# Performance work log

Hardware: AMD Instinct MI355X
Metric: run time of the kernel (lower is better)

## Reference

```python
import jax, jax.numpy as jnp
import numpy as np

D_MODEL = 1024
N_HEADS = 16
DEPTH = D_MODEL // N_HEADS
NEG_INF = -1.0e9


def setup_inputs() -> dict:
    key = jax.random.key(0)
    ks = jax.random.split(key, 11)
    B, S = 2, 2048
    xk = jax.random.normal(ks[0], (B, S, D_MODEL), jnp.float32)
    xq = jax.random.normal(ks[1], (B, S, D_MODEL), jnp.float32)
    xv = jax.random.normal(ks[2], (B, S, D_MODEL), jnp.float32)
    sc = 1.0 / np.sqrt(D_MODEL)
    wq = jax.random.normal(ks[3], (D_MODEL, D_MODEL), jnp.float32) * sc
    wk = jax.random.normal(ks[4], (D_MODEL, D_MODEL), jnp.float32) * sc
    wv = jax.random.normal(ks[5], (D_MODEL, D_MODEL), jnp.float32) * sc
    wo = jax.random.normal(ks[6], (D_MODEL, D_MODEL), jnp.float32) * sc
    bq = jnp.zeros((D_MODEL,), jnp.float32)
    bk = jnp.zeros((D_MODEL,), jnp.float32)
    bv = jnp.zeros((D_MODEL,), jnp.float32)
    bo = jnp.zeros((D_MODEL,), jnp.float32)
    return {"xk": xk, "xq": xq, "xv": xv, "wq": wq, "bq": bq, "wk": wk,
            "bk": bk, "wv": wv, "bv": bv, "wo": wo, "bo": bo}


def _split_heads(t):
    # [B, S, D] -> [B, H, S, depth]
    B, S, _ = t.shape
    return t.reshape(B, S, N_HEADS, DEPTH).transpose(0, 2, 1, 3)


def reference(xk, xq, xv, wq, bq, wk, bk, wv, bv, wo, bo):
    B, Sq, _ = xq.shape
    Sk = xk.shape[1]
    q = _split_heads(xq @ wq + bq)  # [B,H,Sq,d]
    k = _split_heads(xk @ wk + bk)  # [B,H,Sk,d]
    v = _split_heads(xv @ wv + bv)  # [B,H,Sk,d]
    logits = jnp.einsum('bhqd,bhkd->bhqk', q, k) / jnp.sqrt(
        jnp.asarray(DEPTH, q.dtype))
    # additive causal mask: (1 - lower_triangular) * -1e9
    causal = (1.0 - jnp.tril(jnp.ones((Sq, Sk), logits.dtype))) * NEG_INF
    logits = logits + causal[None, None, :, :]
    attn = jax.nn.softmax(logits, axis=-1)
    out = jnp.einsum('bhqk,bhkd->bhqd', attn, v)
    out = out.transpose(0, 2, 1, 3).reshape(B, Sq, D_MODEL)
    return out @ wo + bo
```

## Files before the change

### kernel.cpp

```cpp
#include <hip/hip_runtime.h>

typedef unsigned short u16;
typedef u16 u16x8 __attribute__((ext_vector_type(8)));
typedef __bf16 bf16x8 __attribute__((ext_vector_type(8)));
typedef float f32x4 __attribute__((ext_vector_type(4)));

#define DM 1024
#define SEQ 2048
#define BATCH 2
#define MROWS 4096

__device__ __forceinline__ u16 f2bf(float f) {
  unsigned int x = __builtin_bit_cast(unsigned int, f);
  x += 0x7fffu + ((x >> 16) & 1u);
  return (u16)(x >> 16);
}
__device__ __forceinline__ u16 f2bf_trunc(float f) {
  return (u16)(__builtin_bit_cast(unsigned int, f) >> 16);
}

__device__ __forceinline__ void gld16(const void* g, void* l) {
  __builtin_amdgcn_global_load_lds(
      (const __attribute__((address_space(1))) void*)g,
      (__attribute__((address_space(3))) void*)l, 16, 0, 0);
}

struct TrArgs { const float* in[4]; u16* out[4]; };

__global__ __launch_bounds__(256) void transpose_w4(TrArgs a) {
  const float* __restrict__ in = a.in[blockIdx.z];
  u16* __restrict__ out = a.out[blockIdx.z];
  __shared__ u16 T[64][72];
  int r0 = blockIdx.y * 64, c0 = blockIdx.x * 64;
  int t = threadIdx.x;
  int r = t >> 3, cg = (t & 7) * 8;
#pragma unroll
  for (int p = 0; p < 2; p++) {
    const float* src = in + (size_t)(r0 + r + p * 32) * DM + c0 + cg;
    f32x4 x0 = *(const f32x4*)src;
    f32x4 x1 = *(const f32x4*)(src + 4);
    u16x8 v;
#pragma unroll
    for (int j = 0; j < 4; j++) { v[j] = f2bf(x0[j]); v[4 + j] = f2bf(x1[j]); }
    *(u16x8*)(&T[r + p * 32][cg]) = v;
  }
  __syncthreads();
#pragma unroll
  for (int p = 0; p < 2; p++) {
    int orow = r + p * 32;
    u16x8 v;
#pragma unroll
    for (int j = 0; j < 8; j++) v[j] = T[cg + j][orow];
    *(u16x8*)(out + (size_t)(c0 + orow) * DM + r0 + cg) = v;
  }
}

struct CastArgs { const float* in[3]; u16* out[3]; };

__global__ __launch_bounds__(256) void cast_x(CastArgs a) {
  const float* __restrict__ in = a.in[blockIdx.y];
  u16* __restrict__ out = a.out[blockIdx.y];
  size_t e = ((size_t)blockIdx.x * 256 + threadIdx.x) * 8;
  f32x4 a0 = *(const f32x4*)(in + e);
  f32x4 a1 = *(const f32x4*)(in + e + 4);
  u16x8 v;
#pragma unroll
  for (int j = 0; j < 4; j++) { v[j] = f2bf(a0[j]); v[4 + j] = f2bf(a1[j]); }
  *(u16x8*)(out + e) = v;
}

struct GemmArgs { const void* A[3]; const u16* WT[3]; const float* bias[3]; void* C[3]; };

template <int MT, int NT, bool AF32, bool OF32>
__global__ __launch_bounds__(256) void gemmT(GemmArgs g) {
  __shared__ __align__(16) u16 As[MT * 32 * 32];
  __shared__ __align__(16) u16 Bs[NT * 32 * 32];
  const int z = blockIdx.z;
  const u16* __restrict__ WT = g.WT[z];
  const int tid = threadIdx.x;
  const int lane = tid & 63, wave = tid >> 6;
  const int fr = lane & 15, kq = lane >> 4;
  const int mq = (wave >> 1) * (MT * 16), nq = (wave & 1) * (NT * 16);
  const int m0 = blockIdx.y * (MT * 32), n0 = blockIdx.x * (NT * 32);
  const int srow = tid >> 2;
  const int scA = ((tid & 3) ^ ((srow >> 1) & 3)) * 8;
  const int fco = ((kq ^ ((fr >> 1) & 3)) * 8);
  f32x4 acc[MT][NT] = {};

  for (int kk = 0; kk < DM; kk += 32) {
    __syncthreads();
    if constexpr (AF32) {
      const float* A = (const float*)g.A[z];
#pragma unroll
      for (int i = 0; i < MT / 2; i++) {
        const float* s0 = A + (size_t)(m0 + i * 64 + srow) * DM + kk + scA;
        f32x4 a0 = *(const f32x4*)s0, a1 = *(const f32x4*)(s0 + 4);
        u16x8 v;
#pragma unroll
        for (int j = 0; j < 4; j++) { v[j] = f2bf(a0[j]); v[4 + j] = f2bf(a1[j]); }
        *(u16x8*)(As + (i * 256 + tid) * 8) = v;
      }
    } else {
      const u16* A = (const u16*)g.A[z];
#pragma unroll
      for (int i = 0; i < MT / 2; i++)
        gld16(A + (size_t)(m0 + i * 64 + srow) * DM + kk + scA,
              As + (i * 256 + tid) * 8);
    }
#pragma unroll
    for (int i = 0; i < NT / 2; i++)
      gld16(WT + (size_t)(n0 + i * 64 + srow) * DM + kk + scA,
            Bs + (i * 256 + tid) * 8);
    __syncthreads();
    bf16x8 af[MT], bfr[NT];
#pragma unroll
    for (int mt = 0; mt < MT; mt++)
      af[mt] = __builtin_bit_cast(
          bf16x8, *(const u16x8*)(As + (mq + mt * 16 + fr) * 32 + fco));
#pragma unroll
    for (int nt = 0; nt < NT; nt++)
      bfr[nt] = __builtin_bit_cast(
          bf16x8, *(const u16x8*)(Bs + (nq + nt * 16 + fr) * 32 + fco));
#pragma unroll
    for (int mt = 0; mt < MT; mt++)
#pragma unroll
      for (int nt = 0; nt < NT; nt++)
        acc[mt][nt] =
            __builtin_amdgcn_mfma_f32_16x16x32_bf16(af[mt], bfr[nt], acc[mt][nt], 0, 0, 0);
  }
  const float* __restrict__ bias = g.bias[z];
#pragma unroll
  for (int nt = 0; nt < NT; nt++) {
    int col = n0 + nq + nt * 16 + fr;
    float bb = bias[col];
#pragma unroll
    for (int mt = 0; mt < MT; mt++)
#pragma unroll
      for (int r = 0; r < 4; r++) {
        int row = m0 + mq + mt * 16 + kq * 4 + r;
        float val = acc[mt][nt][r] + bb;
        if constexpr (OF32)
          ((float*)g.C[z])[(size_t)row * DM + col] = val;
        else
          ((u16*)g.C[z])[(size_t)row * DM + col] = f2bf(val);
      }
  }
}

#define KS 72
__global__ __launch_bounds__(256) void attn3(u16* __restrict__ Q,
                                             const u16* __restrict__ K,
                                             const u16* __restrict__ V) {
  __shared__ __align__(16) u16 Ksh[64 * 64];
  __shared__ __align__(16) u16 Vt[80 * KS];
  __shared__ __align__(16) u16 Ps[4][16 * KS];
  const int tid = threadIdx.x, wave = tid >> 6, lane = tid & 63;
  const int fr = lane & 15, kq = lane >> 4;
  const int b = blockIdx.x >> 4, h = blockIdx.x & 15;
  const int qt = 31 - blockIdx.y;
  const float C1 = 0.125f * 1.44269504f;

#pragma unroll
  for (int i = 0; i < 4; i++) {
    int e = tid * 4 + i;
    int rr = e >> 6, cc = e & 63;
    Vt[(64 + rr) * KS + cc] = (rr == 0) ? (u16)0x3F80 : (u16)0;
  }

  const int krow = tid >> 3;
  const int kcs = ((tid & 7) ^ (krow & 7)) * 8;
  const int f7 = fr & 7;
  const int x0 = (kq ^ f7) * 8;
  const int x1 = ((4 + kq) ^ f7) * 8;

  bf16x8 qf0, qf1;
  {
    size_t qr = (size_t)(b * SEQ + qt * 64 + wave * 16 + fr) * DM + h * 64;
    qf0 = __builtin_bit_cast(bf16x8, *(const u16x8*)(Q + qr + kq * 8));
    qf1 = __builtin_bit_cast(bf16x8, *(const u16x8*)(Q + qr + 32 + kq * 8));
  }

  f32x4 ov[5] = {};
  u16* Pw = Ps[wave];

  for (int t = 0; t <= qt; t++) {
    __syncthreads();
    {
      size_t gk = (size_t)(b * SEQ + t * 64 + krow) * DM + h * 64 + kcs;
      gld16(K + gk, Ksh + tid * 8);
      gld16(K + gk + (size_t)32 * DM, Ksh + (256 + tid) * 8);
      size_t gv = (size_t)(b * SEQ + t * 64 + lane) * DM + h * 64 + wave * 16;
      u16x8 v0 = *(const u16x8*)(V + gv);
      u16x8 v1 = *(const u16x8*)(V + gv + 8);
#pragma unroll
      for (int j = 0; j < 8; j++) {
        Vt[(wave * 16 + j) * KS + lane] = v0[j];
        Vt[(wave * 16 + 8 + j) * KS + lane] = v1[j];
      }
    }
    __syncthreads();
    f32x4 sv[4];
#pragma unroll
    for (int nt = 0; nt < 4; nt++) {
      f32x4 s = {};
      bf16x8 b0 = __builtin_bit_cast(
          bf16x8, *(const u16x8*)(Ksh + (nt * 16 + fr) * 64 + x0));
      s = __builtin_amdgcn_mfma_f32_16x16x32_bf16(qf0, b0, s, 0, 0, 0);
      bf16x8 b1 = __builtin_bit_cast(
          bf16x8, *(const u16x8*)(Ksh + (nt * 16 + fr) * 64 + x1));
      s = __builtin_amdgcn_mfma_f32_16x16x32_bf16(qf1, b1, s, 0, 0, 0);
      sv[nt] = s;
    }
    if (t == qt) {
#pragma unroll
      for (int nt = 0; nt < 4; nt++)
#pragma unroll
        for (int r = 0; r < 4; r++)
          if (nt * 16 + fr > wave * 16 + kq * 4 + r) sv[nt][r] = -1e30f;
    }
#pragma unroll
    for (int nt = 0; nt < 4; nt++)
#pragma unroll
      for (int r = 0; r < 4; r++) {
        float pp = __builtin_amdgcn_exp2f(sv[nt][r] * C1);
        Pw[(kq * 4 + r) * KS + nt * 16 + fr] = f2bf_trunc(pp);
      }
#pragma unroll
    for (int kk = 0; kk < 2; kk++) {
      bf16x8 pa = __builtin_bit_cast(
          bf16x8, *(const u16x8*)(Pw + fr * KS + kk * 32 + kq * 8));
#pragma unroll
      for (int nt = 0; nt < 5; nt++) {
        bf16x8 vb = __builtin_bit_cast(
            bf16x8, *(const u16x8*)(Vt + (nt * 16 + fr) * KS + kk * 32 + kq * 8));
        ov[nt] = __builtin_amdgcn_mfma_f32_16x16x32_bf16(pa, vb, ov[nt], 0, 0, 0);
      }
    }
  }
  float rinv[4];
#pragma unroll
  for (int r = 0; r < 4; r++) rinv[r] = 1.0f / __shfl(ov[4][r], lane & 48);
#pragma unroll
  for (int nt = 0; nt < 4; nt++)
#pragma unroll
    for (int r = 0; r < 4; r++) {
      int row = qt * 64 + wave * 16 + kq * 4 + r;
      Q[(size_t)(b * SEQ + row) * DM + h * 64 + nt * 16 + fr] =
          f2bf(ov[nt][r] * rinv[r]);
    }
}

extern "C" void kernel_launch(void* const* d_in, const int* in_sizes, int n_in,
                              void* d_out, int out_size, void* d_ws,
                              size_t ws_size, hipStream_t stream) {
  const float* xk = (const float*)d_in[0];
  const float* xq = (const float*)d_in[1];
  const float* xv = (const float*)d_in[2];
  const float* wq = (const float*)d_in[3];
  const float* bq = (const float*)d_in[4];
  const float* wk = (const float*)d_in[5];
  const float* bk = (const float*)d_in[6];
  const float* wv = (const float*)d_in[7];
  const float* bv = (const float*)d_in[8];
  const float* wo = (const float*)d_in[9];
  const float* bo = (const float*)d_in[10];

  u16* Qb = (u16*)d_ws;
  u16* Kb = Qb + (size_t)MROWS * DM;
  u16* Vb = Kb + (size_t)MROWS * DM;
  u16* WTq = Vb + (size_t)MROWS * DM;
  u16* WTk = WTq + (size_t)DM * DM;
  u16* WTv = WTk + (size_t)DM * DM;
  u16* WTo = WTv + (size_t)DM * DM;
  u16* Xq = WTo + (size_t)DM * DM;
  u16* Xk = Xq + (size_t)MROWS * DM;
  u16* Xv = Xk + (size_t)MROWS * DM;
  const bool cast_path =
      ws_size >= ((size_t)(3 * 8 + 4 * 2 + 3 * 8)) * 1024 * 1024;

  dim3 blk(256);

  TrArgs tr;
  tr.in[0] = wq; tr.in[1] = wk; tr.in[2] = wv; tr.in[3] = wo;
  tr.out[0] = WTq; tr.out[1] = WTk; tr.out[2] = WTv; tr.out[3] = WTo;
  transpose_w4<<<dim3(16, 16, 4), blk, 0, stream>>>(tr);

  GemmArgs gq;
  gq.WT[0] = WTq; gq.WT[1] = WTk; gq.WT[2] = WTv;
  gq.bias[0] = bq; gq.bias[1] = bk; gq.bias[2] = bv;
  gq.C[0] = Qb; gq.C[1] = Kb; gq.C[2] = Vb;
  if (cast_path) {
    CastArgs ca;
    ca.in[0] = xq; ca.in[1] = xk; ca.in[2] = xv;
    ca.out[0] = Xq; ca.out[1] = Xk; ca.out[2] = Xv;
    cast_x<<<dim3(MROWS * DM / 2048, 3), blk, 0, stream>>>(ca);
    gq.A[0] = Xq; gq.A[1] = Xk; gq.A[2] = Xv;
    gemmT<4, 4, false, false>
        <<<dim3(DM / 128, MROWS / 128, 3), blk, 0, stream>>>(gq);
  } else {
    gq.A[0] = xq; gq.A[1] = xk; gq.A[2] = xv;
    gemmT<4, 4, true, false>
        <<<dim3(DM / 128, MROWS / 128, 3), blk, 0, stream>>>(gq);
  }

  attn3<<<dim3(BATCH * 16, 32), blk, 0, stream>>>(Qb, Kb, Vb);

  GemmArgs go;
  go.A[0] = Qb;  go.WT[0] = WTo; go.bias[0] = bo; go.C[0] = d_out;
  go.A[1] = Qb;  go.WT[1] = WTo; go.bias[1] = bo; go.C[1] = d_out;
  go.A[2] = Qb;  go.WT[2] = WTo; go.bias[2] = bo; go.C[2] = d_out;
  gemmT<2, 4, false, true>
      <<<dim3(DM / 128, MROWS / 64, 1), blk, 0, stream>>>(go);
}
```

Before: 224.1 us.

## Emit transposed V from projection GEMM and restructure attention to 128-thread blocks

The QKV projection GEMM now uses a configurable K-tile (64) and writes V directly in a per-head transposed layout. The attention kernel can then load V with async global-to-LDS copies instead of scalar LDS transposes. The attention kernel is rewritten with 2 waves, each handling 32 query rows. It computes S^T so probabilities can be packed with perm into LDS, and it accumulates row sums with shuffles instead of an extra ones-column in V. The output GEMM is retiled to 64x64 blocks. The trade-offs are scattered 2-byte strided stores for transposed V and fewer threads per attention block.

```diff
diff --git a/kernel.cpp b/kernel.cpp
--- a/kernel.cpp
+++ b/kernel.cpp
@@ -1,7 +1,9 @@
 #include <hip/hip_runtime.h>
 
 typedef unsigned short u16;
+typedef unsigned int u32;
 typedef u16 u16x8 __attribute__((ext_vector_type(8)));
+typedef u32 u32x2 __attribute__((ext_vector_type(2)));
 typedef __bf16 bf16x8 __attribute__((ext_vector_type(8)));
 typedef float f32x4 __attribute__((ext_vector_type(4)));
 
@@ -15,8 +17,10 @@
   x += 0x7fffu + ((x >> 16) & 1u);
   return (u16)(x >> 16);
 }
-__device__ __forceinline__ u16 f2bf_trunc(float f) {
-  return (u16)(__builtin_bit_cast(unsigned int, f) >> 16);
+
+__device__ __forceinline__ u32 pack2bf(float lo, float hi) {
+  return __builtin_amdgcn_perm(__builtin_bit_cast(u32, hi),
+                               __builtin_bit_cast(u32, lo), 0x07060302u);
 }
 
 __device__ __forceinline__ void gld16(const void* g, void* l) {
@@ -71,64 +75,77 @@
 
 struct GemmArgs { const void* A[3]; const u16* WT[3]; const float* bias[3]; void* C[3]; };
 
-template <int MT, int NT, bool AF32, bool OF32>
+template <int MT, int NT, int BK, bool AF32, bool OF32, bool VT>
 __global__ __launch_bounds__(256) void gemmT(GemmArgs g) {
-  __shared__ __align__(16) u16 As[MT * 32 * 32];
-  __shared__ __align__(16) u16 Bs[NT * 32 * 32];
+  constexpr int CH = BK / 8;
+  constexpr int CM = CH - 1;
+  constexpr int SH = (CH == 4) ? 1 : 0;
+  __shared__ __align__(16) u16 As[MT * 32 * BK];
+  __shared__ __align__(16) u16 Bs[NT * 32 * BK];
   const int z = blockIdx.z;
   const u16* __restrict__ WT = g.WT[z];
-  const int tid = threadIdx.x;
-  const int lane = tid & 63, wave = tid >> 6;
+  const int tid = threadIdx.x, lane = tid & 63, wave = tid >> 6;
   const int fr = lane & 15, kq = lane >> 4;
   const int mq = (wave >> 1) * (MT * 16), nq = (wave & 1) * (NT * 16);
   const int m0 = blockIdx.y * (MT * 32), n0 = blockIdx.x * (NT * 32);
-  const int srow = tid >> 2;
-  const int scA = ((tid & 3) ^ ((srow >> 1) & 3)) * 8;
-  const int fco = ((kq ^ ((fr >> 1) & 3)) * 8);
+  const int fsel = (fr >> SH) & CM;
   f32x4 acc[MT][NT] = {};
 
-  for (int kk = 0; kk < DM; kk += 32) {
+  for (int kk = 0; kk < DM; kk += BK) {
     __syncthreads();
+    constexpr int AI = MT * 32 * CH / 256;
+    constexpr int BI = NT * 32 * CH / 256;
     if constexpr (AF32) {
       const float* A = (const float*)g.A[z];
 #pragma unroll
-      for (int i = 0; i < MT / 2; i++) {
-        const float* s0 = A + (size_t)(m0 + i * 64 + srow) * DM + kk + scA;
+      for (int i = 0; i < AI; i++) {
+        int ci = i * 256 + tid, row = ci / CH, sl = ci % CH;
+        int sc = (sl ^ ((row >> SH) & CM)) * 8;
+        const float* s0 = A + (size_t)(m0 + row) * DM + kk + sc;
         f32x4 a0 = *(const f32x4*)s0, a1 = *(const f32x4*)(s0 + 4);
         u16x8 v;
 #pragma unroll
         for (int j = 0; j < 4; j++) { v[j] = f2bf(a0[j]); v[4 + j] = f2bf(a1[j]); }
-        *(u16x8*)(As + (i * 256 + tid) * 8) = v;
+        *(u16x8*)(As + ci * 8) = v;
       }
     } else {
       const u16* A = (const u16*)g.A[z];
 #pragma unroll
-      for (int i = 0; i < MT / 2; i++)
-        gld16(A + (size_t)(m0 + i * 64 + srow) * DM + kk + scA,
-              As + (i * 256 + tid) * 8);
-    }
-#pragma unroll
-    for (int i = 0; i < NT / 2; i++)
-      gld16(WT + (size_t)(n0 + i * 64 + srow) * DM + kk + scA,
-            Bs + (i * 256 + tid) * 8);
+      for (int i = 0; i < AI; i++) {
+        int ci = i * 256 + tid, row = ci / CH, sl = ci % CH;
+        int sc = (sl ^ ((row >> SH) & CM)) * 8;
+        gld16(A + (size_t)(m0 + row) * DM + kk + sc, As + ci * 8);
+      }
+    }
+#pragma unroll
+    for (int i = 0; i < BI; i++) {
+      int ci = i * 256 + tid, row = ci / CH, sl = ci % CH;
+      int sc = (sl ^ ((row >> SH) & CM)) * 8;
+      gld16(WT + (size_t)(n0 + row) * DM + kk + sc, Bs + ci * 8);
+    }
     __syncthreads();
-    bf16x8 af[MT], bfr[NT];
-#pragma unroll
-    for (int mt = 0; mt < MT; mt++)
-      af[mt] = __builtin_bit_cast(
-          bf16x8, *(const u16x8*)(As + (mq + mt * 16 + fr) * 32 + fco));
-#pragma unroll
-    for (int nt = 0; nt < NT; nt++)
-      bfr[nt] = __builtin_bit_cast(
-          bf16x8, *(const u16x8*)(Bs + (nq + nt * 16 + fr) * 32 + fco));
-#pragma unroll
-    for (int mt = 0; mt < MT; mt++)
+#pragma unroll
+    for (int kc = 0; kc < BK / 32; kc++) {
+      bf16x8 af[MT], bfr[NT];
+      const int fo = ((kc * 4 + kq) ^ fsel) * 8;
+#pragma unroll
+      for (int mt = 0; mt < MT; mt++)
+        af[mt] = __builtin_bit_cast(
+            bf16x8, *(const u16x8*)(As + (mq + mt * 16 + fr) * BK + fo));
 #pragma unroll
       for (int nt = 0; nt < NT; nt++)
-        acc[mt][nt] =
-            __builtin_amdgcn_mfma_f32_16x16x32_bf16(af[mt], bfr[nt], acc[mt][nt], 0, 0, 0);
+        bfr[nt] = __builtin_bit_cast(
+            bf16x8, *(const u16x8*)(Bs + (nq + nt * 16 + fr) * BK + fo));
+#pragma unroll
+      for (int mt = 0; mt < MT; mt++)
+#pragma unroll
+        for (int nt = 0; nt < NT; nt++)
+          acc[mt][nt] = __builtin_amdgcn_mfma_f32_16x16x32_bf16(
+              af[mt], bfr[nt], acc[mt][nt], 0, 0, 0);
+    }
   }
   const float* __restrict__ bias = g.bias[z];
+  const bool vtr = VT && (z == 2);
 #pragma unroll
   for (int nt = 0; nt < NT; nt++) {
     int col = n0 + nq + nt * 16 + fr;
@@ -139,115 +156,156 @@
       for (int r = 0; r < 4; r++) {
         int row = m0 + mq + mt * 16 + kq * 4 + r;
         float val = acc[mt][nt][r] + bb;
-        if constexpr (OF32)
+        if constexpr (OF32) {
           ((float*)g.C[z])[(size_t)row * DM + col] = val;
-        else
-          ((u16*)g.C[z])[(size_t)row * DM + col] = f2bf(val);
-      }
-  }
-}
-
-#define KS 72
-__global__ __launch_bounds__(256) void attn3(u16* __restrict__ Q,
+        } else {
+          u16* C = (u16*)g.C[z];
+          if (vtr) {
+            size_t idx = ((size_t)((row >> 11) * 16 + (col >> 6)) * 64 +
+                          (col & 63)) * SEQ + (row & 2047);
+            C[idx] = f2bf(val);
+          } else {
+            C[(size_t)row * DM + col] = f2bf(val);
+          }
+        }
+      }
+  }
+}
+
+__global__ __launch_bounds__(128) void attn4(u16* __restrict__ Q,
                                              const u16* __restrict__ K,
-                                             const u16* __restrict__ V) {
+                                             const u16* __restrict__ Vtg) {
   __shared__ __align__(16) u16 Ksh[64 * 64];
-  __shared__ __align__(16) u16 Vt[80 * KS];
-  __shared__ __align__(16) u16 Ps[4][16 * KS];
-  const int tid = threadIdx.x, wave = tid >> 6, lane = tid & 63;
-  const int fr = lane & 15, kq = lane >> 4;
-  const int b = blockIdx.x >> 4, h = blockIdx.x & 15;
+  __shared__ __align__(16) u16 Vsh[64 * 64];
+  __shared__ __align__(16) u16 Psh[64 * 64];
+  __shared__ float Lbuf[2][32];
+  const int tid = threadIdx.x, wq = tid >> 6, lane = tid & 63;
+  const int fr = lane & 15, kq = lane >> 4, f7 = fr & 7;
+  const int bh = blockIdx.x, b = bh >> 4, h = bh & 15;
   const int qt = 31 - blockIdx.y;
   const float C1 = 0.125f * 1.44269504f;
 
+  int xo[2];
+  xo[0] = (kq ^ f7) * 8;
+  xo[1] = ((4 + kq) ^ f7) * 8;
+
+  const u16* kp[4];
+  const u16* vp[4];
 #pragma unroll
   for (int i = 0; i < 4; i++) {
-    int e = tid * 4 + i;
-    int rr = e >> 6, cc = e & 63;
-    Vt[(64 + rr) * KS + cc] = (rr == 0) ? (u16)0x3F80 : (u16)0;
-  }
-
-  const int krow = tid >> 3;
-  const int kcs = ((tid & 7) ^ (krow & 7)) * 8;
-  const int f7 = fr & 7;
-  const int x0 = (kq ^ f7) * 8;
-  const int x1 = ((4 + kq) ^ f7) * 8;
-
-  bf16x8 qf0, qf1;
-  {
-    size_t qr = (size_t)(b * SEQ + qt * 64 + wave * 16 + fr) * DM + h * 64;
-    qf0 = __builtin_bit_cast(bf16x8, *(const u16x8*)(Q + qr + kq * 8));
-    qf1 = __builtin_bit_cast(bf16x8, *(const u16x8*)(Q + qr + 32 + kq * 8));
-  }
-
-  f32x4 ov[5] = {};
-  u16* Pw = Ps[wave];
+    int ci = i * 128 + tid, row = ci >> 3, sl = ci & 7;
+    int sc = (sl ^ (row & 7)) * 8;
+    kp[i] = K + (size_t)(b * SEQ + row) * DM + h * 64 + sc;
+    vp[i] = Vtg + (size_t)(bh * 64 + row) * SEQ + sc;
+  }
+
+  bf16x8 qf[2][2];
+#pragma unroll
+  for (int qtl = 0; qtl < 2; qtl++) {
+    size_t qr = (size_t)(b * SEQ + qt * 64 + wq * 32 + qtl * 16 + fr) * DM + h * 64;
+#pragma unroll
+    for (int kk = 0; kk < 2; kk++)
+      qf[qtl][kk] =
+          __builtin_bit_cast(bf16x8, *(const u16x8*)(Q + qr + kk * 32 + kq * 8));
+  }
+
+  f32x4 ov[2][4] = {};
+  float lac[2] = {0.f, 0.f};
 
   for (int t = 0; t <= qt; t++) {
     __syncthreads();
-    {
-      size_t gk = (size_t)(b * SEQ + t * 64 + krow) * DM + h * 64 + kcs;
-      gld16(K + gk, Ksh + tid * 8);
-      gld16(K + gk + (size_t)32 * DM, Ksh + (256 + tid) * 8);
-      size_t gv = (size_t)(b * SEQ + t * 64 + lane) * DM + h * 64 + wave * 16;
-      u16x8 v0 = *(const u16x8*)(V + gv);
-      u16x8 v1 = *(const u16x8*)(V + gv + 8);
-#pragma unroll
-      for (int j = 0; j < 8; j++) {
-        Vt[(wave * 16 + j) * KS + lane] = v0[j];
-        Vt[(wave * 16 + 8 + j) * KS + lane] = v1[j];
-      }
+#pragma unroll
+    for (int i = 0; i < 4; i++) {
+      int ci = i * 128 + tid;
+      gld16(kp[i] + (size_t)t * 64 * DM, Ksh + ci * 8);
+      gld16(vp[i] + t * 64, Vsh + ci * 8);
     }
     __syncthreads();
-    f32x4 sv[4];
-#pragma unroll
-    for (int nt = 0; nt < 4; nt++) {
-      f32x4 s = {};
-      bf16x8 b0 = __builtin_bit_cast(
-          bf16x8, *(const u16x8*)(Ksh + (nt * 16 + fr) * 64 + x0));
-      s = __builtin_amdgcn_mfma_f32_16x16x32_bf16(qf0, b0, s, 0, 0, 0);
-      bf16x8 b1 = __builtin_bit_cast(
-          bf16x8, *(const u16x8*)(Ksh + (nt * 16 + fr) * 64 + x1));
-      s = __builtin_amdgcn_mfma_f32_16x16x32_bf16(qf1, b1, s, 0, 0, 0);
-      sv[nt] = s;
+
+    f32x4 st[2][4];
+#pragma unroll
+    for (int kt = 0; kt < 4; kt++) {
+      bf16x8 k0 = __builtin_bit_cast(
+          bf16x8, *(const u16x8*)(Ksh + (kt * 16 + fr) * 64 + xo[0]));
+      bf16x8 k1 = __builtin_bit_cast(
+          bf16x8, *(const u16x8*)(Ksh + (kt * 16 + fr) * 64 + xo[1]));
+#pragma unroll
+      for (int qtl = 0; qtl < 2; qtl++) {
+        f32x4 s = {};
+        s = __builtin_amdgcn_mfma_f32_16x16x32_bf16(k0, qf[qtl][0], s, 0, 0, 0);
+        s = __builtin_amdgcn_mfma_f32_16x16x32_bf16(k1, qf[qtl][1], s, 0, 0, 0);
+        st[qtl][kt] = s;
+      }
     }
     if (t == qt) {
 #pragma unroll
-      for (int nt = 0; nt < 4; nt++)
-#pragma unroll
-        for (int r = 0; r < 4; r++)
-          if (nt * 16 + fr > wave * 16 + kq * 4 + r) sv[nt][r] = -1e30f;
-    }
+      for (int qtl = 0; qtl < 2; qtl++)
+#pragma unroll
+        for (int kt = 0; kt < 4; kt++)
+#pragma unroll
+          for (int r = 0; r < 4; r++)
+            if (kt * 16 + kq * 4 + r > wq * 32 + qtl * 16 + fr)
+              st[qtl][kt][r] = -1e30f;
+    }
+#pragma unroll
+    for (int qtl = 0; qtl < 2; qtl++) {
+      float ls = 0.f;
+      int prow = (wq * 32 + qtl * 16 + fr) * 64;
+#pragma unroll
+      for (int kt = 0; kt < 4; kt++) {
+        float p0 = __builtin_amdgcn_exp2f(st[qtl][kt][0] * C1);
+        float p1 = __builtin_amdgcn_exp2f(st[qtl][kt][1] * C1);
+        float p2 = __builtin_amdgcn_exp2f(st[qtl][kt][2] * C1);
+        float p3 = __builtin_amdgcn_exp2f(st[qtl][kt][3] * C1);
+        ls += (p0 + p1) + (p2 + p3);
+        u32x2 d;
+        d[0] = pack2bf(p0, p1);
+        d[1] = pack2bf(p2, p3);
+        int sl = (2 * kt + (kq >> 1)) ^ f7;
+        *(u32x2*)(Psh + prow + sl * 8 + (kq & 1) * 4) = d;
+      }
+      ls += __shfl_xor(ls, 16);
+      ls += __shfl_xor(ls, 32);
+      lac[qtl] += ls;
+    }
+#pragma unroll
+    for (int kk = 0; kk < 2; kk++) {
+      bf16x8 pa[2];
+#pragma unroll
+      for (int qtl = 0; qtl < 2; qtl++)
+        pa[qtl] = __builtin_bit_cast(
+            bf16x8,
+            *(const u16x8*)(Psh + (wq * 32 + qtl * 16 + fr) * 64 + xo[kk]));
+#pragma unroll
+      for (int nt = 0; nt < 4; nt++) {
+        bf16x8 vb = __builtin_bit_cast(
+            bf16x8, *(const u16x8*)(Vsh + (nt * 16 + fr) * 64 + xo[kk]));
+#pragma unroll
+        for (int qtl = 0; qtl < 2; qtl++)
+          ov[qtl][nt] = __builtin_amdgcn_mfma_f32_16x16x32_bf16(
+              pa[qtl], vb, ov[qtl][nt], 0, 0, 0);
+      }
+    }
+  }
+  if (kq == 0) {
+    Lbuf[wq][fr] = lac[0];
+    Lbuf[wq][16 + fr] = lac[1];
+  }
+#pragma unroll
+  for (int qtl = 0; qtl < 2; qtl++) {
+    float rinv[4];
+#pragma unroll
+    for (int r = 0; r < 4; r++)
+      rinv[r] = 1.0f / Lbuf[wq][qtl * 16 + kq * 4 + r];
 #pragma unroll
     for (int nt = 0; nt < 4; nt++)
 #pragma unroll
       for (int r = 0; r < 4; r++) {
-        float pp = __builtin_amdgcn_exp2f(sv[nt][r] * C1);
-        Pw[(kq * 4 + r) * KS + nt * 16 + fr] = f2bf_trunc(pp);
-      }
-#pragma unroll
-    for (int kk = 0; kk < 2; kk++) {
-      bf16x8 pa = __builtin_bit_cast(
-          bf16x8, *(const u16x8*)(Pw + fr * KS + kk * 32 + kq * 8));
-#pragma unroll
-      for (int nt = 0; nt < 5; nt++) {
-        bf16x8 vb = __builtin_bit_cast(
-            bf16x8, *(const u16x8*)(Vt + (nt * 16 + fr) * KS + kk * 32 + kq * 8));
-        ov[nt] = __builtin_amdgcn_mfma_f32_16x16x32_bf16(pa, vb, ov[nt], 0, 0, 0);
-      }
-    }
-  }
-  float rinv[4];
-#pragma unroll
-  for (int r = 0; r < 4; r++) rinv[r] = 1.0f / __shfl(ov[4][r], lane & 48);
-#pragma unroll
-  for (int nt = 0; nt < 4; nt++)
-#pragma unroll
-    for (int r = 0; r < 4; r++) {
-      int row = qt * 64 + wave * 16 + kq * 4 + r;
-      Q[(size_t)(b * SEQ + row) * DM + h * 64 + nt * 16 + fr] =
-          f2bf(ov[nt][r] * rinv[r]);
-    }
+        int row = qt * 64 + wq * 32 + qtl * 16 + kq * 4 + r;
+        Q[(size_t)(b * SEQ + row) * DM + h * 64 + nt * 16 + fr] =
+            f2bf(ov[qtl][nt][r] * rinv[r]);
+      }
+  }
 }
 
 extern "C" void kernel_launch(void* const* d_in, const int* in_sizes, int n_in,
@@ -295,20 +353,20 @@
     ca.out[0] = Xq; ca.out[1] = Xk; ca.out[2] = Xv;
     cast_x<<<dim3(MROWS * DM / 2048, 3), blk, 0, stream>>>(ca);
     gq.A[0] = Xq; gq.A[1] = Xk; gq.A[2] = Xv;
-    gemmT<4, 4, false, false>
+    gemmT<4, 4, 64, false, false, true>
         <<<dim3(DM / 128, MROWS / 128, 3), blk, 0, stream>>>(gq);
   } else {
     gq.A[0] = xq; gq.A[1] = xk; gq.A[2] = xv;
-    gemmT<4, 4, true, false>
+    gemmT<4, 4, 64, true, false, true>
         <<<dim3(DM / 128, MROWS / 128, 3), blk, 0, stream>>>(gq);
   }
 
-  attn3<<<dim3(BATCH * 16, 32), blk, 0, stream>>>(Qb, Kb, Vb);
+  attn4<<<dim3(BATCH * 16, 32), dim3(128), 0, stream>>>(Qb, Kb, Vb);
 
   GemmArgs go;
-  go.A[0] = Qb;  go.WT[0] = WTo; go.bias[0] = bo; go.C[0] = d_out;
-  go.A[1] = Qb;  go.WT[1] = WTo; go.bias[1] = bo; go.C[1] = d_out;
-  go.A[2] = Qb;  go.WT[2] = WTo; go.bias[2] = bo; go.C[2] = d_out;
-  gemmT<2, 4, false, true>
-      <<<dim3(DM / 128, MROWS / 64, 1), blk, 0, stream>>>(go);
-}
+  go.A[0] = Qb; go.WT[0] = WTo; go.bias[0] = bo; go.C[0] = d_out;
+  go.A[1] = Qb; go.WT[1] = WTo; go.bias[1] = bo; go.C[1] = d_out;
+  go.A[2] = Qb; go.WT[2] = WTo; go.bias[2] = bo; go.C[2] = d_out;
+  gemmT<2, 2, 64, false, true, false>
+      <<<dim3(DM / 64, MROWS / 64, 1), blk, 0, stream>>>(go);
+}
```

Measured after the change: 240.9 us. +7.5%, slower.
